# Optimization experiments

Hardware: AMD Instinct MI355X
Metric: run time of the kernel (lower is better)

## Reference

```python
import jax, jax.numpy as jnp
import numpy as np
from jax import lax

B, N, CIN, COUT, R, K = 4, 16384, 64, 128, 32, 3
VOX_EPS = 1e-6
BN3D_EPS = 1e-4
BN1D_EPS = 1e-5
LRELU_SLOPE = 0.1


def setup_inputs() -> dict:
    key = jax.random.key(0)
    ks = jax.random.split(key, 20)
    d = {}
    d['features'] = jax.random.normal(ks[0], (B, N, CIN), jnp.float32)
    d['coords'] = jax.random.normal(ks[1], (B, N, 3), jnp.float32)
    # Conv3D #1: (D,H,W,Cin,Cout) + bias
    d['conv1_w'] = jax.random.normal(ks[2], (K, K, K, CIN, COUT), jnp.float32) * 0.02
    d['conv1_b'] = jax.random.normal(ks[3], (COUT,), jnp.float32) * 0.02
    d['bn1_g'] = jax.random.uniform(ks[4], (COUT,), jnp.float32, 0.75, 1.25)
    d['bn1_b'] = jax.random.normal(ks[5], (COUT,), jnp.float32) * 0.1
    d['bn1_m'] = jax.random.normal(ks[6], (COUT,), jnp.float32) * 0.1
    d['bn1_v'] = jax.random.uniform(ks[7], (COUT,), jnp.float32, 0.5, 1.5)
    # Conv3D #2
    d['conv2_w'] = jax.random.normal(ks[8], (K, K, K, COUT, COUT), jnp.float32) * 0.02
    d['conv2_b'] = jax.random.normal(ks[9], (COUT,), jnp.float32) * 0.02
    d['bn2_g'] = jax.random.uniform(ks[10], (COUT,), jnp.float32, 0.75, 1.25)
    d['bn2_b'] = jax.random.normal(ks[11], (COUT,), jnp.float32) * 0.1
    d['bn2_m'] = jax.random.normal(ks[12], (COUT,), jnp.float32) * 0.1
    d['bn2_v'] = jax.random.uniform(ks[13], (COUT,), jnp.float32, 0.5, 1.5)
    # Point SharedMLP: Conv1D k=1 -> matmul, + BN + ReLU
    d['pw'] = jax.random.normal(ks[14], (CIN, COUT), jnp.float32) * 0.05
    d['pb'] = jax.random.normal(ks[15], (COUT,), jnp.float32) * 0.02
    d['pbn_g'] = jax.random.uniform(ks[16], (COUT,), jnp.float32, 0.75, 1.25)
    d['pbn_b'] = jax.random.normal(ks[17], (COUT,), jnp.float32) * 0.1
    d['pbn_m'] = jax.random.normal(ks[18], (COUT,), jnp.float32) * 0.1
    d['pbn_v'] = jax.random.uniform(ks[19], (COUT,), jnp.float32, 0.5, 1.5)
    return d


def _bn(x, g, b, m, v, eps):
    return (x - m) * (g * lax.rsqrt(v + eps)) + b


def _leaky_relu(x):
    return jnp.where(x >= 0, x, LRELU_SLOPE * x)


def _pvconv(features, coords, conv1_w, conv1_b, bn1_g, bn1_b, bn1_m, bn1_v,
            conv2_w, conv2_b, bn2_g, bn2_b, bn2_m, bn2_v,
            pw, pb, pbn_g, pbn_b, pbn_m, pbn_v):
    r = R
    # ---- Voxelization (normalize coords, scatter-average into grid) ----
    c = lax.stop_gradient(coords)                                   # (B,N,3)
    nc = c - jnp.mean(c, axis=1, keepdims=True)
    denom = jnp.max(jnp.linalg.norm(nc, axis=2, keepdims=True), axis=1, keepdims=True) * 2.0 + VOX_EPS
    nc = nc / denom + 0.5
    nc = jnp.clip(nc * r, 0.0, r - 1)                                # (B,N,3) in [0, r-1]
    vox = jnp.round(nc).astype(jnp.int32)                            # (B,N,3)

    batch_off = jnp.arange(B, dtype=jnp.int32)[:, None] * (r * r * r)
    lin = batch_off + vox[..., 0] * (r * r) + vox[..., 1] * r + vox[..., 2]  # (B,N)
    lin = lin.reshape(-1)
    feat_flat = features.reshape(-1, CIN)
    sums = jax.ops.segment_sum(feat_flat, lin, num_segments=B * r * r * r)   # (B*r^3,Cin)
    cnts = jax.ops.segment_sum(jnp.ones((B * N,), jnp.float32), lin, num_segments=B * r * r * r)
    cnts = jnp.where(cnts == 0, 1.0, cnts)
    grid = (sums / cnts[:, None]).reshape(B, r, r, r, CIN)           # (B,r,r,r,Cin)

    # ---- Voxel branch: Conv3D -> BN -> LeakyReLU (x2) ----
    dn = ('NDHWC', 'DHWIO', 'NDHWC')
    g = lax.conv_general_dilated(grid, conv1_w, (1, 1, 1), 'SAME', dimension_numbers=dn) + conv1_b
    g = _leaky_relu(_bn(g, bn1_g, bn1_b, bn1_m, bn1_v, BN3D_EPS))
    g = lax.conv_general_dilated(g, conv2_w, (1, 1, 1), 'SAME', dimension_numbers=dn) + conv2_b
    g = _leaky_relu(_bn(g, bn2_g, bn2_b, bn2_m, bn2_v, BN3D_EPS))    # (B,r,r,r,Cout)

    # ---- Trilinear devoxelize: gather 8 corners with interpolation weights ----
    g_flat = g.reshape(B, r * r * r, COUT)
    c0 = jnp.floor(nc).astype(jnp.int32)                             # (B,N,3)
    frac = nc - c0.astype(nc.dtype)
    c1 = jnp.minimum(c0 + 1, r - 1)
    vox_pts = jnp.zeros((B, N, COUT), jnp.float32)
    for dx in (0, 1):
        for dy in (0, 1):
            for dz in (0, 1):
                ix = c1[..., 0] if dx else c0[..., 0]
                iy = c1[..., 1] if dy else c0[..., 1]
                iz = c1[..., 2] if dz else c0[..., 2]
                w = ((frac[..., 0] if dx else 1.0 - frac[..., 0]) *
                     (frac[..., 1] if dy else 1.0 - frac[..., 1]) *
                     (frac[..., 2] if dz else 1.0 - frac[..., 2]))   # (B,N)
                idx = ix * (r * r) + iy * r + iz                      # (B,N)
                gathered = jnp.take_along_axis(g_flat, idx[..., None], axis=1)  # (B,N,Cout)
                vox_pts = vox_pts + w[..., None] * gathered

    # ---- Point branch: SharedMLP (1x1 conv -> BN -> ReLU) ----
    pf = jnp.einsum('bnc,cd->bnd', features, pw) + pb
    pf = jax.nn.relu(_bn(pf, pbn_g, pbn_b, pbn_m, pbn_v, BN1D_EPS))

    return vox_pts + pf                                              # (B,N,Cout)


def reference(features, coords, conv1_w, conv1_b, bn1_g, bn1_b, bn1_m, bn1_v,
              conv2_w, conv2_b, bn2_g, bn2_b, bn2_m, bn2_v,
              pw, pb, pbn_g, pbn_b, pbn_m, pbn_v):
    fused = _pvconv(features, coords, conv1_w, conv1_b, bn1_g, bn1_b, bn1_m, bn1_v,
                    conv2_w, conv2_b, bn2_g, bn2_b, bn2_m, bn2_v,
                    pw, pb, pbn_g, pbn_b, pbn_m, pbn_v)
    return (fused, coords)
```

## Files before the change

kernel.cpp:

```cpp
#include <hip/hip_runtime.h>
#include <hip/hip_bf16.h>

constexpr int B    = 4;
constexpr int N    = 16384;
constexpr int CIN  = 64;
constexpr int COUT = 128;
constexpr int R    = 32;
constexpr int R3   = R * R * R;
constexpr int RP   = 34;
constexpr int RP3  = RP * RP * RP;
constexpr float VOX_EPS   = 1e-6f;
constexpr float BN3D_EPS  = 1e-4f;
constexpr float BN1D_EPS  = 1e-5f;
constexpr float LRELU     = 0.1f;

typedef __attribute__((ext_vector_type(8))) short bf16x8;
typedef __attribute__((ext_vector_type(4))) float f32x4;
typedef __attribute__((ext_vector_type(8))) unsigned short u16x8;

__device__ inline float bf2f(ushort u) {
    union { unsigned int i; float f; } x; x.i = ((unsigned int)u) << 16; return x.f;
}
__device__ inline ushort f2bf(float f) {
    union { float f; unsigned int i; } x; x.f = f;
    unsigned int r = x.i + 0x7fffu + ((x.i >> 16) & 1u);
    return (ushort)(r >> 16);
}

__device__ inline int swz(int base, int z) {
    return (base ^ (z & 3) ^ ((z >> 2) & 3)) & 3;
}

__global__ __launch_bounds__(256) void k_stats_sum(const float* __restrict__ coords,
                                                   float* __restrict__ stats) {
    int blk = blockIdx.x;
    int b = blk >> 4, stripe = blk & 15;
    const float* c = coords + ((size_t)b * N + stripe * 1024) * 3;
    float sx = 0.f, sy = 0.f, sz = 0.f;
    for (int i = threadIdx.x; i < 1024; i += 256) {
        sx += c[i * 3 + 0];
        sy += c[i * 3 + 1];
        sz += c[i * 3 + 2];
    }
    __shared__ float red[256];
    float vals[3] = {sx, sy, sz};
    for (int k = 0; k < 3; ++k) {
        red[threadIdx.x] = vals[k];
        __syncthreads();
        for (int s = 128; s > 0; s >>= 1) {
            if (threadIdx.x < s) red[threadIdx.x] += red[threadIdx.x + s];
            __syncthreads();
        }
        if (threadIdx.x == 0) atomicAdd(&stats[b * 8 + k], red[0]);
        __syncthreads();
    }
}

__global__ __launch_bounds__(256) void k_stats_max(const float* __restrict__ coords,
                                                   float* __restrict__ stats) {
    int blk = blockIdx.x;
    int b = blk >> 4, stripe = blk & 15;
    const float invN = 1.0f / (float)N;
    float mx = stats[b * 8 + 0] * invN;
    float my = stats[b * 8 + 1] * invN;
    float mz = stats[b * 8 + 2] * invN;
    const float* c = coords + ((size_t)b * N + stripe * 1024) * 3;
    float mm = 0.f;
    for (int i = threadIdx.x; i < 1024; i += 256) {
        float dx = c[i * 3 + 0] - mx;
        float dy = c[i * 3 + 1] - my;
        float dz = c[i * 3 + 2] - mz;
        mm = fmaxf(mm, sqrtf(dx * dx + dy * dy + dz * dz));
    }
    __shared__ float red[256];
    red[threadIdx.x] = mm;
    __syncthreads();
    for (int s = 128; s > 0; s >>= 1) {
        if (threadIdx.x < s) red[threadIdx.x] = fmaxf(red[threadIdx.x], red[threadIdx.x + s]);
        __syncthreads();
    }
    if (threadIdx.x == 0)
        atomicMax((unsigned*)&stats[b * 8 + 3], __float_as_uint(red[0]));
}

__device__ inline void compute_nc(const float* __restrict__ coords,
                                  const float* __restrict__ stats,
                                  int p, int b, float& nx, float& ny, float& nz) {
    const float invN = 1.0f / (float)N;
    float mmax = __uint_as_float(((const unsigned*)stats)[b * 8 + 3]);
    float denom = mmax * 2.0f + VOX_EPS;
    float cx = coords[(size_t)p * 3 + 0];
    float cy = coords[(size_t)p * 3 + 1];
    float cz = coords[(size_t)p * 3 + 2];
    nx = (cx - stats[b * 8 + 0] * invN) / denom + 0.5f;
    ny = (cy - stats[b * 8 + 1] * invN) / denom + 0.5f;
    nz = (cz - stats[b * 8 + 2] * invN) / denom + 0.5f;
    nx = fminf(fmaxf(nx * (float)R, 0.f), (float)(R - 1));
    ny = fminf(fmaxf(ny * (float)R, 0.f), (float)(R - 1));
    nz = fminf(fmaxf(nz * (float)R, 0.f), (float)(R - 1));
}

__global__ __launch_bounds__(256) void k_scatter(const float* __restrict__ coords,
                                                 const float* __restrict__ feats,
                                                 const float* __restrict__ stats,
                                                 float* __restrict__ sums,
                                                 float* __restrict__ cnt) {
    int sub = threadIdx.x >> 6;
    int ci  = threadIdx.x & 63;
    int p   = blockIdx.x * 4 + sub;
    __shared__ int s_lin[4];
    if (ci == 0) {
        int b = p >> 14;
        float nx, ny, nz;
        compute_nc(coords, stats, p, b, nx, ny, nz);
        int vx = (int)rintf(nx);
        int vy = (int)rintf(ny);
        int vz = (int)rintf(nz);
        int lin = ((b * R + vx) * R + vy) * R + vz;
        s_lin[sub] = lin;
        atomicAdd(&cnt[lin], 1.0f);
    }
    __syncthreads();
    atomicAdd(&sums[(size_t)s_lin[sub] * CIN + ci], feats[(size_t)p * CIN + ci]);
}

__global__ __launch_bounds__(256) void k_zero_border(ushort* __restrict__ buf, int nchunks) {
    int i = blockIdx.x * 256 + threadIdx.x;
    if (i >= nchunks) return;
    int v = i >> 2;
    int r = v % RP3;
    int z = r % RP;
    int t = r / RP;
    int y = t % RP;
    int x = (t / RP) % RP;
    if (x == 0 || x == RP - 1 || y == 0 || y == RP - 1 || z == 0 || z == RP - 1)
        *(uint4*)(buf + (size_t)i * 8) = make_uint4(0u, 0u, 0u, 0u);
}

__global__ __launch_bounds__(256) void k_finalize(const float* __restrict__ sums,
                                                  const float* __restrict__ cnt,
                                                  ushort* __restrict__ gridp) {
    int i = blockIdx.x * 256 + threadIdx.x;
    float c = cnt[i >> 6];
    float val = sums[i] / (c == 0.f ? 1.f : c);
    int ci = i & 63;
    int v = i >> 6;
    int vz = v & 31, vy = (v >> 5) & 31, vx = (v >> 10) & 31, b = v >> 15;
    size_t o = ((((size_t)(b * 2 + (ci >> 5)) * RP + vx + 1) * RP + vy + 1) * RP + vz + 1) * 32
               + (ci & 31);
    gridp[o] = f2bf(val);
}

__global__ __launch_bounds__(256) void k_wq(const float* __restrict__ w,
                                            ushort* __restrict__ wq) {
    int idx = blockIdx.x * 256 + threadIdx.x;
    int j    = idx & 7;
    int lane = (idx >> 3) & 63;
    int nt   = (idx >> 9) & 7;
    int g    = idx >> 12;
    int k = g * 32 + ((lane >> 4) << 3) + j;
    int n = nt * 16 + (lane & 15);
    wq[idx] = f2bf(w[(size_t)k * COUT + n]);
}

template <int CI, bool PLANAR_OUT>
__global__ __launch_bounds__(256, 3) void k_conv_mfma(const ushort* __restrict__ in,
                                                      const ushort* __restrict__ wq,
                                                      const float* __restrict__ bias,
                                                      const float* __restrict__ bng,
                                                      const float* __restrict__ bnb,
                                                      const float* __restrict__ bnm,
                                                      const float* __restrict__ bnv,
                                                      ushort* __restrict__ out) {
    constexpr int NCHI = CI / 32;
    __shared__ __align__(16) ushort sl[18 * RP * 32];

    int bid = blockIdx.x;
    int Y = bid & 7;
    int x = (bid >> 3) & 31;
    int b = bid >> 8;
    int y0 = Y * 4;
    int tid = threadIdx.x;
    int wave = tid >> 6, lane = tid & 63, quad = lane >> 4, l16 = lane & 15;
    int wm = wave >> 1, wn = wave & 1;

    f32x4 acc[4][4] = {};

    for (int cc = 0; cc < NCHI; ++cc) {
        const ushort* base = in + (((size_t)(b * NCHI + cc) * RP + x) * RP + y0) * RP * 32;
        __syncthreads();
        for (int t = tid; t < 18 * 136; t += 256) {
            int row = t / 136;
            int g16 = t - row * 136;
            int X = row / 6, Yl = row - X * 6;
            int z = g16 >> 2, ch = g16 & 3;
            uint4 v = *(const uint4*)(base + ((size_t)(X * RP + Yl) * RP) * 32 + g16 * 8);
            *(uint4*)(sl + ((row * RP + z) * 4 + swz(ch, z)) * 8) = v;
        }
        __syncthreads();

        for (int tap = 0; tap < 27; ++tap) {
            int dx = tap / 9, rem = tap - dx * 9;
            int dy = rem / 3, dz = rem - dy * 3;

            const ushort* bp = wq + ((size_t)((tap * NCHI + cc) * 8 + wn * 4) * 64 + lane) * 8;
            bf16x8 bfr[4], afr[4];
#pragma unroll
            for (int nt = 0; nt < 4; ++nt)
                bfr[nt] = *(const bf16x8*)(bp + nt * 512);
#pragma unroll
            for (int mt = 0; mt < 4; ++mt) {
                int row18 = dx * 6 + wm * 2 + (mt >> 1) + dy;
                int zrow = ((mt & 1) << 4) + l16 + dz;
                afr[mt] = *(const bf16x8*)(sl + ((row18 * RP + zrow) * 4 + swz(quad, zrow)) * 8);
            }
#pragma unroll
            for (int mt = 0; mt < 4; ++mt)
#pragma unroll
                for (int nt = 0; nt < 4; ++nt)
                    acc[mt][nt] = __builtin_amdgcn_mfma_f32_16x16x32_bf16(
                        afr[mt], bfr[nt], acc[mt][nt], 0, 0, 0);
        }
    }

    float sc[4], sb[4], bs[4];
#pragma unroll
    for (int nt = 0; nt < 4; ++nt) {
        int co = wn * 64 + nt * 16 + l16;
        sc[nt] = bng[co] * rsqrtf(bnv[co] + BN3D_EPS);
        sb[nt] = bnb[co] - bnm[co] * sc[nt];
        bs[nt] = bias[co];
    }
#pragma unroll
    for (int mt = 0; mt < 4; ++mt) {
#pragma unroll
        for (int reg = 0; reg < 4; ++reg) {
            int m = wm * 64 + mt * 16 + quad * 4 + reg;
            int i = m >> 5, z = m & 31;
#pragma unroll
            for (int nt = 0; nt < 4; ++nt) {
                float v = (acc[mt][nt][reg] + bs[nt]) * sc[nt] + sb[nt];
                v = v >= 0.f ? v : LRELU * v;
                int co = wn * 64 + nt * 16 + l16;
                if (PLANAR_OUT) {
                    size_t o = ((((size_t)(b * 4 + (co >> 5)) * RP + (x + 1)) * RP
                                 + (y0 + i + 1)) * RP + (z + 1)) * 32 + (co & 31);
                    out[o] = f2bf(v);
                } else {
                    size_t o = (((size_t)(b * R + x) * R + (y0 + i)) * R + z) * COUT + co;
                    out[o] = f2bf(v);
                }
            }
        }
    }
}

__global__ __launch_bounds__(256, 2) void k_devox(const float* __restrict__ coords,
                                                  const float* __restrict__ feats,
                                                  const float* __restrict__ stats,
                                                  const ushort* __restrict__ g2,
                                                  const ushort* __restrict__ pwq,
                                                  const float* __restrict__ pb,
                                                  const float* __restrict__ pg,
                                                  const float* __restrict__ pbb,
                                                  const float* __restrict__ pm,
                                                  const float* __restrict__ pv,
                                                  float* __restrict__ out) {
    __shared__ __align__(16) ushort sfeat[128 * 64];
    __shared__ int   sidx[128 * 8];
    __shared__ float swt[128 * 8];

    int blk = blockIdx.x, tid = threadIdx.x;
    int wave = tid >> 6, lane = tid & 63, quad = lane >> 4, l16 = lane & 15;
    int p0 = blk * 128;

    if (tid < 128) {
        int p = p0 + tid, b = p >> 14;
        float nx, ny, nz;
        compute_nc(coords, stats, p, b, nx, ny, nz);
        int cx0 = (int)floorf(nx), cy0 = (int)floorf(ny), cz0 = (int)floorf(nz);
        float fx = nx - (float)cx0, fy = ny - (float)cy0, fz = nz - (float)cz0;
        int cx1 = min(cx0 + 1, R - 1), cy1 = min(cy0 + 1, R - 1), cz1 = min(cz0 + 1, R - 1);
#pragma unroll
        for (int k = 0; k < 8; ++k) {
            int dx = (k >> 2) & 1, dy = (k >> 1) & 1, dz = k & 1;
            int ix = dx ? cx1 : cx0;
            int iy = dy ? cy1 : cy0;
            int iz = dz ? cz1 : cz0;
            sidx[tid * 8 + k] = (((b * R + ix) * R + iy) * R + iz) * COUT;
            swt[tid * 8 + k] = (dx ? fx : 1.f - fx) * (dy ? fy : 1.f - fy) * (dz ? fz : 1.f - fz);
        }
    }
    for (int i = 0; i < 4; ++i) {
        int c = i * 256 + tid;
        int p = c >> 3, ch = c & 7;
        const float* src = feats + (size_t)(p0 + p) * CIN + ch * 8;
        float4 f0 = *(const float4*)src;
        float4 f1 = *(const float4*)(src + 4);
        u16x8 u;
        u[0] = f2bf(f0.x); u[1] = f2bf(f0.y); u[2] = f2bf(f0.z); u[3] = f2bf(f0.w);
        u[4] = f2bf(f1.x); u[5] = f2bf(f1.y); u[6] = f2bf(f1.z); u[7] = f2bf(f1.w);
        *(u16x8*)&sfeat[(p * 8 + (ch ^ (p & 7))) * 8] = u;
    }
    __syncthreads();

    f32x4 acc[8][2] = {};
#pragma unroll
    for (int cc = 0; cc < 2; ++cc) {
        const ushort* bp = pwq + ((size_t)(cc * 8 + wave * 2) * 64 + lane) * 8;
        bf16x8 b0 = *(const bf16x8*)bp;
        bf16x8 b1 = *(const bf16x8*)(bp + 512);
#pragma unroll
        for (int mt = 0; mt < 8; ++mt) {
            int prow = mt * 16 + l16;
            int ch = cc * 4 + quad;
            bf16x8 a = *(const bf16x8*)&sfeat[(prow * 8 + (ch ^ (prow & 7))) * 8];
            acc[mt][0] = __builtin_amdgcn_mfma_f32_16x16x32_bf16(a, b0, acc[mt][0], 0, 0, 0);
            acc[mt][1] = __builtin_amdgcn_mfma_f32_16x16x32_bf16(a, b1, acc[mt][1], 0, 0, 0);
        }
    }

    int co0 = wave * 32 + l16, co1 = co0 + 16;
    float sc0 = pg[co0] * rsqrtf(pv[co0] + BN1D_EPS);
    float sb0 = pbb[co0] - pm[co0] * sc0;
    float bs0 = pb[co0];
    float sc1 = pg[co1] * rsqrtf(pv[co1] + BN1D_EPS);
    float sb1 = pbb[co1] - pm[co1] * sc1;
    float bs1 = pb[co1];

#pragma unroll
    for (int mt = 0; mt < 8; ++mt) {
#pragma unroll
        for (int reg = 0; reg < 4; ++reg) {
            int pl = mt * 16 + quad * 4 + reg;
            float v0 = fmaxf((acc[mt][0][reg] + bs0) * sc0 + sb0, 0.f);
            float v1 = fmaxf((acc[mt][1][reg] + bs1) * sc1 + sb1, 0.f);
#pragma unroll
            for (int k = 0; k < 8; ++k) {
                int idx = sidx[pl * 8 + k];
                float w = swt[pl * 8 + k];
                v0 += w * bf2f(g2[(size_t)idx + co0]);
                v1 += w * bf2f(g2[(size_t)idx + co1]);
            }
            size_t o = (size_t)(p0 + pl) * COUT;
            out[o + co0] = v0;
            out[o + co1] = v1;
        }
    }
}

extern "C" void kernel_launch(void* const* d_in, const int* in_sizes, int n_in,
                              void* d_out, int out_size, void* d_ws, size_t ws_size,
                              hipStream_t stream) {
    const float* feats   = (const float*)d_in[0];
    const float* coords  = (const float*)d_in[1];
    const float* conv1_w = (const float*)d_in[2];
    const float* conv1_b = (const float*)d_in[3];
    const float* bn1_g   = (const float*)d_in[4];
    const float* bn1_b   = (const float*)d_in[5];
    const float* bn1_m   = (const float*)d_in[6];
    const float* bn1_v   = (const float*)d_in[7];
    const float* conv2_w = (const float*)d_in[8];
    const float* conv2_b = (const float*)d_in[9];
    const float* bn2_g   = (const float*)d_in[10];
    const float* bn2_b   = (const float*)d_in[11];
    const float* bn2_m   = (const float*)d_in[12];
    const float* bn2_v   = (const float*)d_in[13];
    const float* pw      = (const float*)d_in[14];
    const float* pb      = (const float*)d_in[15];
    const float* pbn_g   = (const float*)d_in[16];
    const float* pbn_b   = (const float*)d_in[17];
    const float* pbn_m   = (const float*)d_in[18];
    const float* pbn_v   = (const float*)d_in[19];

    char* p = (char*)d_ws;
    float* stats = (float*)p;                        p += 256;
    float* sums  = (float*)p;                        p += (size_t)B * R3 * CIN * 4;
    float* cnt   = (float*)p;                        p += (size_t)B * R3 * 4;
    ushort* gridp = (ushort*)p;                      p += (size_t)B * 2 * RP3 * 32 * 2;
    ushort* g1p   = (ushort*)p;                      p += (size_t)B * 4 * RP3 * 32 * 2;
    ushort* g2b   = (ushort*)p;                      p += (size_t)B * R3 * COUT * 2;
    ushort* wq1   = (ushort*)p;                      p += 54 * 4096 * 2;
    ushort* wq2   = (ushort*)p;                      p += 108 * 4096 * 2;
    ushort* pwq   = (ushort*)p;                      p += 2 * 4096 * 2;
    float*  outf  = (float*)d_out;

    hipMemsetAsync(stats, 0, 256 + ((size_t)B * R3 * CIN + (size_t)B * R3) * sizeof(float),
                   stream);
    {
        int nc1 = B * 2 * RP3 * 4;
        int nc2 = B * 4 * RP3 * 4;
        k_zero_border<<<(nc1 + 255) / 256, 256, 0, stream>>>(gridp, nc1);
        k_zero_border<<<(nc2 + 255) / 256, 256, 0, stream>>>(g1p, nc2);
    }

    k_stats_sum<<<64, 256, 0, stream>>>(coords, stats);
    k_stats_max<<<64, 256, 0, stream>>>(coords, stats);
    k_scatter<<<(B * N) / 4, 256, 0, stream>>>(coords, feats, stats, sums, cnt);
    k_finalize<<<(B * R3 * CIN) / 256, 256, 0, stream>>>(sums, cnt, gridp);

    k_wq<<<(54 * 4096) / 256, 256, 0, stream>>>(conv1_w, wq1);
    k_wq<<<(108 * 4096) / 256, 256, 0, stream>>>(conv2_w, wq2);
    k_wq<<<(2 * 4096) / 256, 256, 0, stream>>>(pw, pwq);

    k_conv_mfma<CIN, true><<<B * R * (R / 4), 256, 0, stream>>>(
        gridp, wq1, conv1_b, bn1_g, bn1_b, bn1_m, bn1_v, g1p);
    k_conv_mfma<COUT, false><<<B * R * (R / 4), 256, 0, stream>>>(
        g1p, wq2, conv2_b, bn2_g, bn2_b, bn2_m, bn2_v, g2b);

    k_devox<<<(B * N) / 128, 256, 0, stream>>>(coords, feats, stats, g2b, pwq, pb,
                                               pbn_g, pbn_b, pbn_m, pbn_v, outf);

    hipMemcpyAsync(outf + (size_t)B * N * COUT, coords, (size_t)B * N * 3 * sizeof(float),
                   hipMemcpyDeviceToDevice, stream);
}
```

Baseline: 355.7 us.

## Pad conv LDS layout, restructure tap loops, vectorize devox gather, merge setup launches

The conv kernel's LDS tile drops the XOR swizzle in favour of padding each z-row to 5 16-byte slots, which avoids bank conflicts with simpler addressing. The 27-tap loop becomes nested dx/dy/dz loops with the dy/dz loops unrolled and precomputed base pointers. The devox kernel now stages the point-MLP output in LDS as bf16 and then gathers grid rows with 16-byte vector loads and writes float4 stores, replacing scalar per-channel gathers. The three weight-quantize launches and the two border-zero launches are each merged into one. Costs are more LDS in devox, which may lower occupancy, and extra bf16 rounding of the MLP output.

```diff
diff --git a/kernel.cpp b/kernel.cpp
--- a/kernel.cpp
+++ b/kernel.cpp
@@ -25,10 +25,6 @@
     union { float f; unsigned int i; } x; x.f = f;
     unsigned int r = x.i + 0x7fffu + ((x.i >> 16) & 1u);
     return (ushort)(r >> 16);
-}
-
-__device__ inline int swz(int base, int z) {
-    return (base ^ (z & 3) ^ ((z >> 2) & 3)) & 3;
 }
 
 __global__ __launch_bounds__(256) void k_stats_sum(const float* __restrict__ coords,
@@ -151,16 +147,22 @@
     gridp[o] = f2bf(val);
 }
 
-__global__ __launch_bounds__(256) void k_wq(const float* __restrict__ w,
-                                            ushort* __restrict__ wq) {
+__global__ __launch_bounds__(256) void k_wq_all(const float* __restrict__ w1,
+                                                const float* __restrict__ w2,
+                                                const float* __restrict__ pw,
+                                                ushort* __restrict__ wq) {
     int idx = blockIdx.x * 256 + threadIdx.x;
+    int g = idx >> 12;
+    const float* src; int gl;
+    if (g < 54)       { src = w1; gl = g; }
+    else if (g < 162) { src = w2; gl = g - 54; }
+    else              { src = pw; gl = g - 162; }
     int j    = idx & 7;
     int lane = (idx >> 3) & 63;
     int nt   = (idx >> 9) & 7;
-    int g    = idx >> 12;
-    int k = g * 32 + ((lane >> 4) << 3) + j;
+    int k = gl * 32 + ((lane >> 4) << 3) + j;
     int n = nt * 16 + (lane & 15);
-    wq[idx] = f2bf(w[(size_t)k * COUT + n]);
+    wq[idx] = f2bf(src[(size_t)k * COUT + n]);
 }
 
 template <int CI, bool PLANAR_OUT>
@@ -173,7 +175,7 @@
                                                       const float* __restrict__ bnv,
                                                       ushort* __restrict__ out) {
     constexpr int NCHI = CI / 32;
-    __shared__ __align__(16) ushort sl[18 * RP * 32];
+    __shared__ __align__(16) ushort sl[18 * 34 * 5 * 8];
 
     int bid = blockIdx.x;
     int Y = bid & 7;
@@ -191,35 +193,43 @@
         __syncthreads();
         for (int t = tid; t < 18 * 136; t += 256) {
             int row = t / 136;
-            int g16 = t - row * 136;
+            int r   = t - row * 136;
             int X = row / 6, Yl = row - X * 6;
-            int z = g16 >> 2, ch = g16 & 3;
-            uint4 v = *(const uint4*)(base + ((size_t)(X * RP + Yl) * RP) * 32 + g16 * 8);
-            *(uint4*)(sl + ((row * RP + z) * 4 + swz(ch, z)) * 8) = v;
+            uint4 v = *(const uint4*)(base + ((size_t)(X * RP + Yl) * RP) * 32 + r * 8);
+            int z = r >> 2, ch = r & 3;
+            *(uint4*)(sl + ((row * 34 + z) * 5 + ch) * 8) = v;
         }
         __syncthreads();
 
-        for (int tap = 0; tap < 27; ++tap) {
-            int dx = tap / 9, rem = tap - dx * 9;
-            int dy = rem / 3, dz = rem - dy * 3;
-
-            const ushort* bp = wq + ((size_t)((tap * NCHI + cc) * 8 + wn * 4) * 64 + lane) * 8;
-            bf16x8 bfr[4], afr[4];
-#pragma unroll
-            for (int nt = 0; nt < 4; ++nt)
-                bfr[nt] = *(const bf16x8*)(bp + nt * 512);
-#pragma unroll
-            for (int mt = 0; mt < 4; ++mt) {
-                int row18 = dx * 6 + wm * 2 + (mt >> 1) + dy;
-                int zrow = ((mt & 1) << 4) + l16 + dz;
-                afr[mt] = *(const bf16x8*)(sl + ((row18 * RP + zrow) * 4 + swz(quad, zrow)) * 8);
+        const ushort* abase0 = sl + (((wm * 2) * 34 + l16) * 5 + quad) * 8;
+        const ushort* bbase  = wq + (size_t)(cc * 8 + wn * 4) * 512 + lane * 8;
+
+#pragma unroll 1
+        for (int dx = 0; dx < 3; ++dx) {
+            const ushort* abase = abase0 + dx * (6 * 34 * 5 * 8);
+            const ushort* bpx   = bbase + (size_t)dx * 9 * NCHI * 4096;
+#pragma unroll
+            for (int dy = 0; dy < 3; ++dy) {
+#pragma unroll
+                for (int dz = 0; dz < 3; ++dz) {
+                    const ushort* bp = bpx + (size_t)(dy * 3 + dz) * NCHI * 4096;
+                    bf16x8 bfr[4], afr[4];
+#pragma unroll
+                    for (int nt = 0; nt < 4; ++nt)
+                        bfr[nt] = *(const bf16x8*)(bp + nt * 512);
+#pragma unroll
+                    for (int mt = 0; mt < 4; ++mt) {
+                        int off = ((((mt >> 1) + dy) * 34) + (mt & 1) * 16 + dz) * 40;
+                        afr[mt] = *(const bf16x8*)(abase + off);
+                    }
+#pragma unroll
+                    for (int mt = 0; mt < 4; ++mt)
+#pragma unroll
+                        for (int nt = 0; nt < 4; ++nt)
+                            acc[mt][nt] = __builtin_amdgcn_mfma_f32_16x16x32_bf16(
+                                afr[mt], bfr[nt], acc[mt][nt], 0, 0, 0);
+                }
             }
-#pragma unroll
-            for (int mt = 0; mt < 4; ++mt)
-#pragma unroll
-                for (int nt = 0; nt < 4; ++nt)
-                    acc[mt][nt] = __builtin_amdgcn_mfma_f32_16x16x32_bf16(
-                        afr[mt], bfr[nt], acc[mt][nt], 0, 0, 0);
         }
     }
 
@@ -267,6 +277,7 @@
                                                   const float* __restrict__ pv,
                                                   float* __restrict__ out) {
     __shared__ __align__(16) ushort sfeat[128 * 64];
+    __shared__ __align__(16) ushort smlp[128 * 128];
     __shared__ int   sidx[128 * 8];
     __shared__ float swt[128 * 8];
 
@@ -321,31 +332,44 @@
     }
 
     int co0 = wave * 32 + l16, co1 = co0 + 16;
-    float sc0 = pg[co0] * rsqrtf(pv[co0] + BN1D_EPS);
-    float sb0 = pbb[co0] - pm[co0] * sc0;
-    float bs0 = pb[co0];
-    float sc1 = pg[co1] * rsqrtf(pv[co1] + BN1D_EPS);
-    float sb1 = pbb[co1] - pm[co1] * sc1;
-    float bs1 = pb[co1];
-
-#pragma unroll
-    for (int mt = 0; mt < 8; ++mt) {
-#pragma unroll
-        for (int reg = 0; reg < 4; ++reg) {
-            int pl = mt * 16 + quad * 4 + reg;
-            float v0 = fmaxf((acc[mt][0][reg] + bs0) * sc0 + sb0, 0.f);
-            float v1 = fmaxf((acc[mt][1][reg] + bs1) * sc1 + sb1, 0.f);
-#pragma unroll
-            for (int k = 0; k < 8; ++k) {
-                int idx = sidx[pl * 8 + k];
-                float w = swt[pl * 8 + k];
-                v0 += w * bf2f(g2[(size_t)idx + co0]);
-                v1 += w * bf2f(g2[(size_t)idx + co1]);
+    {
+        float sc0 = pg[co0] * rsqrtf(pv[co0] + BN1D_EPS);
+        float sb0 = pbb[co0] - pm[co0] * sc0;
+        float bs0 = pb[co0];
+        float sc1 = pg[co1] * rsqrtf(pv[co1] + BN1D_EPS);
+        float sb1 = pbb[co1] - pm[co1] * sc1;
+        float bs1 = pb[co1];
+#pragma unroll
+        for (int mt = 0; mt < 8; ++mt) {
+#pragma unroll
+            for (int reg = 0; reg < 4; ++reg) {
+                int pl = mt * 16 + quad * 4 + reg;
+                smlp[pl * 128 + co0] = f2bf(fmaxf((acc[mt][0][reg] + bs0) * sc0 + sb0, 0.f));
+                smlp[pl * 128 + co1] = f2bf(fmaxf((acc[mt][1][reg] + bs1) * sc1 + sb1, 0.f));
             }
-            size_t o = (size_t)(p0 + pl) * COUT;
-            out[o + co0] = v0;
-            out[o + co1] = v1;
-        }
+        }
+    }
+    __syncthreads();
+
+#pragma unroll
+    for (int it = 0; it < 8; ++it) {
+        int t = it * 256 + tid;
+        int p = t >> 4, c = t & 15;
+        float a[8];
+        const ushort* m = &smlp[p * 128 + c * 8];
+#pragma unroll
+        for (int j = 0; j < 8; ++j) a[j] = bf2f(m[j]);
+#pragma unroll
+        for (int k = 0; k < 8; ++k) {
+            int idx = sidx[p * 8 + k];
+            float w = swt[p * 8 + k];
+            bf16x8 row = *(const bf16x8*)(g2 + (size_t)idx + c * 8);
+#pragma unroll
+            for (int j = 0; j < 8; ++j) a[j] += w * bf2f(((u16x8)row)[j]);
+        }
+        float* o = out + (size_t)(p0 + p) * COUT + c * 8;
+        *(float4*)o       = make_float4(a[0], a[1], a[2], a[3]);
+        *(float4*)(o + 4) = make_float4(a[4], a[5], a[6], a[7]);
     }
 }
 
@@ -380,18 +404,17 @@
     ushort* gridp = (ushort*)p;                      p += (size_t)B * 2 * RP3 * 32 * 2;
     ushort* g1p   = (ushort*)p;                      p += (size_t)B * 4 * RP3 * 32 * 2;
     ushort* g2b   = (ushort*)p;                      p += (size_t)B * R3 * COUT * 2;
-    ushort* wq1   = (ushort*)p;                      p += 54 * 4096 * 2;
-    ushort* wq2   = (ushort*)p;                      p += 108 * 4096 * 2;
-    ushort* pwq   = (ushort*)p;                      p += 2 * 4096 * 2;
+    ushort* wq    = (ushort*)p;                      p += (size_t)164 * 4096 * 2;
+    ushort* wq1 = wq;
+    ushort* wq2 = wq + 54 * 4096;
+    ushort* pwq = wq + 162 * 4096;
     float*  outf  = (float*)d_out;
 
     hipMemsetAsync(stats, 0, 256 + ((size_t)B * R3 * CIN + (size_t)B * R3) * sizeof(float),
                    stream);
     {
-        int nc1 = B * 2 * RP3 * 4;
-        int nc2 = B * 4 * RP3 * 4;
-        k_zero_border<<<(nc1 + 255) / 256, 256, 0, stream>>>(gridp, nc1);
-        k_zero_border<<<(nc2 + 255) / 256, 256, 0, stream>>>(g1p, nc2);
+        int nc = B * 6 * RP3 * 4;
+        k_zero_border<<<(nc + 255) / 256, 256, 0, stream>>>(gridp, nc);
     }
 
     k_stats_sum<<<64, 256, 0, stream>>>(coords, stats);
@@ -399,9 +422,7 @@
     k_scatter<<<(B * N) / 4, 256, 0, stream>>>(coords, feats, stats, sums, cnt);
     k_finalize<<<(B * R3 * CIN) / 256, 256, 0, stream>>>(sums, cnt, gridp);
 
-    k_wq<<<(54 * 4096) / 256, 256, 0, stream>>>(conv1_w, wq1);
-    k_wq<<<(108 * 4096) / 256, 256, 0, stream>>>(conv2_w, wq2);
-    k_wq<<<(2 * 4096) / 256, 256, 0, stream>>>(pw, pwq);
+    k_wq_all<<<(164 * 4096) / 256, 256, 0, stream>>>(conv1_w, conv2_w, pw, wq);
 
     k_conv_mfma<CIN, true><<<B * R * (R / 4), 256, 0, stream>>>(
         gridp, wq1, conv1_b, bn1_g, bn1_b, bn1_m, bn1_v, g1p);
```

Result: no change. 356.3 us (+0.2%).
